# Kernel optimization log

Hardware: AMD Instinct MI355X
Metric: run time of the kernel (lower is better)

Reference implementation:

```python
import jax, jax.numpy as jnp
import numpy as np

C = 128        # in_channels
N = 80000      # nodes per type (user, item)
E = 1000000    # edges per relation
L = 400000     # link labels


def _evolve_gcn(x_src, edge_index, n_dst, p, W0, Wih, Whh, bih, bhh):
    """EvolveGCNH layer: TopK pooling -> 1-step GRU weight evolution -> GCN."""
    # TopK pooling: score = x @ p / ||p||, keep top C nodes, gate by tanh(score)
    score = x_src @ p / (jnp.linalg.norm(p) + 1e-16)          # [N_src]
    top_vals, top_idx = jax.lax.top_k(score, x_src.shape[1])   # k = C
    X_tilde = x_src[top_idx] * jnp.tanh(top_vals)[:, None]     # [C, C]
    # One GRU step: 'batch' dim = C rows of X_tilde, hidden = current weight W0
    gi = X_tilde @ Wih.T + bih                                 # [C, 3C]
    gh = W0 @ Whh.T + bhh                                      # [C, 3C]
    i_r, i_z, i_n = jnp.split(gi, 3, axis=1)
    h_r, h_z, h_n = jnp.split(gh, 3, axis=1)
    r = jax.nn.sigmoid(i_r + h_r)
    z = jax.nn.sigmoid(i_z + h_z)
    n = jnp.tanh(i_n + r * h_n)
    W = (1.0 - z) * n + z * W0                                 # evolved weight [C, C]
    # GCN propagation with symmetric degree norm, no self loops
    xw = x_src @ W                                             # [N_src, C]
    row, col = edge_index[0], edge_index[1]
    ones = jnp.ones(row.shape[0], dtype=xw.dtype)
    deg_src = jax.ops.segment_sum(ones, row, num_segments=x_src.shape[0])
    deg_dst = jax.ops.segment_sum(ones, col, num_segments=n_dst)
    inv_s = jnp.where(deg_src > 0, jax.lax.rsqrt(jnp.maximum(deg_src, 1.0)), 0.0)
    inv_d = jnp.where(deg_dst > 0, jax.lax.rsqrt(jnp.maximum(deg_dst, 1.0)), 0.0)
    norm = inv_s[row] * inv_d[col]                             # [E]
    return jax.ops.segment_sum(xw[row] * norm[:, None], col, num_segments=n_dst)


def setup_inputs() -> dict:
    key = jax.random.key(0)
    ks = jax.random.split(key, 20)
    f = lambda i, shape, s: jax.random.normal(ks[i], shape, dtype=jnp.float32) * s
    s_w = 1.0 / np.sqrt(C)
    return {
        "x_user": f(0, (N, C), 1.0),
        "x_item": f(1, (N, C), 1.0),
        "edge_ui": jax.random.randint(ks[2], (2, E), 0, N),
        "edge_iu": jax.random.randint(ks[3], (2, E), 0, N),
        "edge_label_index": jax.random.randint(ks[4], (2, L), 0, N),
        "p_ui": f(5, (C,), s_w),
        "W0_ui": f(6, (C, C), s_w),
        "Wih_ui": f(7, (3 * C, C), s_w),
        "Whh_ui": f(8, (3 * C, C), s_w),
        "bih_ui": f(9, (3 * C,), s_w),
        "bhh_ui": f(10, (3 * C,), s_w),
        "p_iu": f(11, (C,), s_w),
        "W0_iu": f(12, (C, C), s_w),
        "Wih_iu": f(13, (3 * C, C), s_w),
        "Whh_iu": f(14, (3 * C, C), s_w),
        "bih_iu": f(15, (3 * C,), s_w),
        "bhh_iu": f(16, (3 * C,), s_w),
        "W_post": f(17, (C, 2), s_w),
        "b_post": f(18, (2,), s_w),
    }


def reference(x_user, x_item, edge_ui, edge_iu, edge_label_index,
              p_ui, W0_ui, Wih_ui, Whh_ui, bih_ui, bhh_ui,
              p_iu, W0_iu, Wih_iu, Whh_iu, bih_iu, bhh_iu,
              W_post, b_post):
    # HeteroConv: one EvolveGCNH per relation, outputs grouped by dst node type
    h_item = jax.nn.relu(_evolve_gcn(x_user, edge_ui, x_item.shape[0],
                                     p_ui, W0_ui, Wih_ui, Whh_ui, bih_ui, bhh_ui))
    h_user = jax.nn.relu(_evolve_gcn(x_item, edge_iu, x_user.shape[0],
                                     p_iu, W0_iu, Wih_iu, Whh_iu, bih_iu, bhh_iu))
    # Link scorer: gather endpoints, hadamard, linear(C->2), sum over last dim
    h_src = h_user[edge_label_index[0]]                        # [L, C]
    h_dst = h_item[edge_label_index[1]]                        # [L, C]
    h = (h_src * h_dst) @ W_post + b_post                      # [L, 2]
    return jnp.sum(h, axis=-1)                                 # [L]
```

## Files before the change

### kernel.cpp

```cpp
#include <hip/hip_runtime.h>
#include <hip/hip_fp16.h>

constexpr int KC    = 128;
constexpr int NBLK  = 2048;
constexpr int CAPA  = 1024;
constexpr int CBITS = 12;
constexpr int CSZ   = 1 << CBITS;

using half8   = __attribute__((ext_vector_type(8))) _Float16;
using float4v = __attribute__((ext_vector_type(4))) float;

__device__ __forceinline__ unsigned fkey(float s) {
  unsigned u = __float_as_uint(s);
  return (u & 0x80000000u) ? ~u : (u | 0x80000000u);
}

__global__ __launch_bounds__(256) void m1_cnt_scores(
    const int* __restrict__ eui, const int* __restrict__ eiu,
    unsigned* __restrict__ cnts,
    const float* __restrict__ xu, const float* __restrict__ xi,
    const float* __restrict__ pu, const float* __restrict__ pi,
    float* __restrict__ scores, unsigned* __restrict__ hist,
    __half* __restrict__ x16,
    int E, int N, int NBC, int chunk, int NTOT) {
  __shared__ unsigned hD[4 * 48], hS[4 * 48];
  int t = threadIdx.x;
  if (blockIdx.x < NBLK) {
    int blk = blockIdx.x, w = t >> 6;
    for (int b = t; b < 4 * 48; b += 256) { hD[b] = 0; hS[b] = 0; }
    __syncthreads();
    int lo = blk * chunk, hi = min(2 * E, lo + chunk);
    for (int i = lo + t; i < hi; i += 256) {
      int rel = i >= E;
      const int* e = rel ? eiu : eui;
      int j = i - rel * E;
      atomicAdd(&hD[w * 48 + ((rel * N + e[E + j]) >> CBITS)], 1u);
      atomicAdd(&hS[w * 48 + ((rel * N + e[j]) >> CBITS)], 1u);
    }
    __syncthreads();
    for (int b = t; b < NBC; b += 256) {
      cnts[(size_t)blk * NBC + b] = hD[b] + hD[48 + b] + hD[96 + b] + hD[144 + b];
      cnts[(size_t)NTOT + (size_t)blk * NBC + b] =
          hS[b] + hS[48 + b] + hS[96 + b] + hS[144 + b];
    }
  } else {
    int gw = (blockIdx.x - NBLK) * 8 + (t >> 5);
    if (gw >= 2 * N) return;
    int lane = t & 31;
    int rel = gw >= N;
    int r = gw - rel * N;
    const float* x = rel ? xi : xu;
    const float* p = rel ? pi : pu;
    float4 xv = ((const float4*)(x + (size_t)r * KC))[lane];
    float4 pv = ((const float4*)p)[lane];
    __half2 h0 = __floats2half2_rn(xv.x, xv.y);
    __half2 h1 = __floats2half2_rn(xv.z, xv.w);
    uint2 u; u.x = *(unsigned*)&h0; u.y = *(unsigned*)&h1;
    ((uint2*)(x16 + (size_t)gw * KC))[lane] = u;
    float s = xv.x * pv.x + xv.y * pv.y + xv.z * pv.z + xv.w * pv.w;
#pragma unroll
    for (int off = 16; off; off >>= 1) s += __shfl_down(s, off, 32);
    if (lane == 0) {
      scores[gw] = s;
      atomicAdd(&hist[rel * 65536 + (fkey(s) >> 16)], 1u);
    }
  }
}

__global__ __launch_bounds__(1024) void m2_thresh_scan1(
    const unsigned* __restrict__ cnts, unsigned* __restrict__ sc,
    unsigned* __restrict__ bsum, const unsigned* __restrict__ hist,
    unsigned* __restrict__ ctrl, int NTOT, int NBC, int SCB) {
  __shared__ __align__(16) unsigned smem[1024 + 64 + 2];
  int t = threadIdx.x;
  if (blockIdx.x < 2) {
    const unsigned* h = hist + blockIdx.x * 65536;
    unsigned* c = ctrl + blockIdx.x * 8;
    unsigned* csum = smem;
    unsigned* bs = smem + 1024;
    unsigned s = 0;
    int hi = 65536 - 64 * t;
    for (int b = hi - 64; b < hi; ++b) s += h[b];
    csum[t] = s;
    __syncthreads();
    for (int off = 1; off < 1024; off <<= 1) {
      unsigned add = (t >= off) ? csum[t - off] : 0;
      __syncthreads();
      csum[t] += add;
      __syncthreads();
    }
    unsigned above = (t == 0) ? 0u : csum[t - 1];
    if (csum[t] >= 128u && above < 128u) { smem[1088] = (unsigned)t; smem[1089] = above; }
    __syncthreads();
    int chi = 65536 - 64 * (int)smem[1088];
    unsigned s_above = smem[1089];
    if (t < 64) bs[t] = h[chi - 1 - t];
    __syncthreads();
    if (t < 64) {
      unsigned v = bs[t], cum = v;
#pragma unroll
      for (int off = 1; off < 64; off <<= 1) {
        unsigned u = __shfl_up(cum, off, 64);
        if (t >= off) cum += u;
      }
      unsigned prev = cum - v;
      if (s_above + cum >= 128u && s_above + prev < 128u)
        c[0] = (unsigned)(chi - 1 - t);
    }
  } else {
    int vb = blockIdx.x - 2;
    unsigned* sh = smem;
    int seg = vb / SCB, lb = vb % SCB;
    int li = lb * 1024 + t;
    unsigned v = 0;
    if (li < NTOT) {
      int b = li >> 11, blk = li & (NBLK - 1);
      v = cnts[(size_t)seg * NTOT + (size_t)blk * NBC + b];
    }
    sh[t] = v; __syncthreads();
    for (int off = 1; off < 1024; off <<= 1) {
      unsigned add = (t >= off) ? sh[t - off] : 0;
      __syncthreads();
      sh[t] += add;
      __syncthreads();
    }
    if (li < NTOT) sc[(size_t)seg * NTOT + li] = sh[t] - v;
    if (t == 1023) bsum[vb] = sh[1023];
  }
}

__global__ __launch_bounds__(256) void m3_scan2_compact(
    unsigned* __restrict__ bsum, int nb,
    const float* __restrict__ scores, unsigned* __restrict__ ctrl,
    int* __restrict__ cand_idx, float* __restrict__ cand_val, int N) {
  if (blockIdx.x < 2) {
    __shared__ unsigned sh[256];
    unsigned* bs = bsum + blockIdx.x * nb;
    int t = threadIdx.x;
    unsigned v = (t < nb) ? bs[t] : 0;
    sh[t] = v; __syncthreads();
    for (int off = 1; off < 256; off <<= 1) {
      unsigned add = (t >= off) ? sh[t - off] : 0;
      __syncthreads();
      sh[t] += add;
      __syncthreads();
    }
    if (t < nb) bs[t] = sh[t] - v;
  } else {
    int i = (blockIdx.x - 2) * 256 + threadIdx.x;
    if (i >= 2 * N) return;
    int rel = i >= N;
    float s = scores[i];
    if ((fkey(s) >> 16) >= ctrl[rel * 8]) {
      unsigned pos = atomicAdd(&ctrl[rel * 8 + 1], 1u);
      if (pos < 2048u) {
        cand_idx[rel * 2048 + pos] = i - rel * N;
        cand_val[rel * 2048 + pos] = s;
      }
    }
  }
}

__global__ __launch_bounds__(256) void m4_topk_part(
    const int* __restrict__ eui, const int* __restrict__ eiu,
    const unsigned* __restrict__ cnts, const unsigned* __restrict__ sc,
    const unsigned* __restrict__ bsum,
    unsigned* __restrict__ recsD, unsigned* __restrict__ recsS,
    const unsigned* __restrict__ ctrl,
    const int* __restrict__ cand_idx, const float* __restrict__ cand_val,
    const float* __restrict__ pu, const float* __restrict__ pi,
    int* __restrict__ top_idx, float* __restrict__ top_tanh,
    int E, int N, int NBC, int chunk, int NTOT, int SCB) {
  __shared__ __align__(16) char smem[16896];
  int t = threadIdx.x;
  if (blockIdx.x < 2) {
    float* vals = (float*)smem;
    int*   idxs = (int*)(smem + 8192);
    float* red  = (float*)(smem + 16384);
    int rel = blockIdx.x;
    const float* p = rel ? pi : pu;
    int n = (int)ctrl[rel * 8 + 1]; if (n > 2048) n = 2048;
    for (int i = t; i < n; i += 256) {
      vals[i] = cand_val[rel * 2048 + i];
      idxs[i] = cand_idx[rel * 2048 + i];
    }
    if (t < 128) { float pv = p[t]; red[t] = pv * pv; }
    __syncthreads();
    for (int off = 64; off; off >>= 1) {
      if (t < off) red[t] += red[t + off];
      __syncthreads();
    }
    float pn = sqrtf(red[0]) + 1e-16f;
    for (int c = t; c < n; c += 256) {
      float v = vals[c]; int id = idxs[c];
      int rank = 0;
      for (int j = 0; j < n; ++j) {
        float vj = vals[j];
        rank += (vj > v) || (vj == v && idxs[j] < id);
      }
      if (rank < KC) {
        top_idx[rel * KC + rank] = id;
        top_tanh[rel * KC + rank] = tanhf(v / pn);
      }
    }
  } else {
    unsigned* curD   = (unsigned*)smem;
    unsigned* curS   = (unsigned*)(smem + 256);
    unsigned* deltaD = (unsigned*)(smem + 512);
    unsigned* deltaS = (unsigned*)(smem + 768);
    unsigned* stageD = (unsigned*)(smem + 1024);
    unsigned* stageS = (unsigned*)(smem + 5120);
    unsigned char* bktD = (unsigned char*)(smem + 9216);
    unsigned char* bktS = (unsigned char*)(smem + 10240);
    int blk = blockIdx.x - 2;
    if (t < 64) {
      unsigned v = (t < NBC) ? cnts[(size_t)blk * NBC + t] : 0;
      unsigned cum = v;
#pragma unroll
      for (int off = 1; off < 64; off <<= 1) {
        unsigned u = __shfl_up(cum, off, 64);
        if (t >= off) cum += u;
      }
      if (t < NBC) curD[t] = cum - v;
    } else if (t < 128) {
      int l = t - 64;
      unsigned v = (l < NBC) ? cnts[(size_t)NTOT + (size_t)blk * NBC + l] : 0;
      unsigned cum = v;
#pragma unroll
      for (int off = 1; off < 64; off <<= 1) {
        unsigned u = __shfl_up(cum, off, 64);
        if (l >= off) cum += u;
      }
      if (l < NBC) curS[l] = cum - v;
    }
    __syncthreads();
    if (t < NBC) {
      int li = t * NBLK + blk;
      deltaD[t] = sc[li] + bsum[li >> 10] - curD[t];
      deltaS[t] = sc[NTOT + li] + bsum[SCB + (li >> 10)] - curS[t];
    }
    __syncthreads();
    int lo = blk * chunk, hi = min(2 * E, lo + chunk);
    for (int i = lo + t; i < hi; i += 256) {
      int rel = i >= E;
      const int* e = rel ? eiu : eui;
      int j = i - rel * E;
      int src_g = rel * N + e[j];
      int dst_g = rel * N + e[E + j];
      int bD = dst_g >> CBITS;
      unsigned pD = atomicAdd(&curD[bD], 1u);
      stageD[pD] = (unsigned)src_g | ((unsigned)(dst_g & (CSZ - 1)) << 18);
      bktD[pD] = (unsigned char)bD;
      int bS = src_g >> CBITS;
      unsigned pS = atomicAdd(&curS[bS], 1u);
      stageS[pS] = (unsigned)(src_g & (CSZ - 1));
      bktS[pS] = (unsigned char)bS;
    }
    __syncthreads();
    int cnt = hi - lo;
    for (int j = t; j < cnt; j += 256) {
      recsD[deltaD[bktD[j]] + j] = stageD[j];
      recsS[deltaS[bktS[j]] + j] = stageS[j];
    }
  }
}

__global__ __launch_bounds__(1024) void m5_refine_gru(
    const unsigned* __restrict__ sc, const unsigned* __restrict__ bsum,
    const unsigned* __restrict__ recsD, const unsigned* __restrict__ recsS,
    int* __restrict__ ssrc, int* __restrict__ deg_dst, int* __restrict__ endp,
    int* __restrict__ deg_src,
    const float* __restrict__ xu, const float* __restrict__ xi,
    const int* __restrict__ top_idx, const float* __restrict__ top_tanh,
    const float* __restrict__ W0u, const float* __restrict__ W0i,
    const float* __restrict__ Wihu, const float* __restrict__ Wihi,
    const float* __restrict__ Whhu, const float* __restrict__ Whhi,
    const float* __restrict__ bihu, const float* __restrict__ bihi,
    const float* __restrict__ bhhu, const float* __restrict__ bhhi,
    __half* __restrict__ Wt,
    int E, int NBC, int N2, int NTOT, int SCB) {
  __shared__ __align__(16) char smem[32832];
  int t = threadIdx.x;
  if ((int)blockIdx.x < 2 * NBC) {
    unsigned* rh  = (unsigned*)smem;
    unsigned* cur = (unsigned*)(smem + 16384);
    unsigned* t16 = (unsigned*)(smem + 32768);
    int isS = blockIdx.x >= NBC;
    int c = blockIdx.x - (isS ? NBC : 0);
    size_t soff = isS ? (size_t)NTOT : 0;
    int bso = isS ? SCB : 0;
    int liLo = c * NBLK;
    int lo = (int)(sc[soff + liLo] + bsum[bso + (liLo >> 10)]);
    int hi;
    if (c + 1 < NBC) {
      int liHi = (c + 1) * NBLK;
      hi = (int)(sc[soff + liHi] + bsum[bso + (liHi >> 10)]);
    } else hi = 2 * E;
    for (int b = t; b < CSZ; b += 1024) rh[b] = 0;
    __syncthreads();
    if (isS) {
      for (int j = lo + t; j < hi; j += 1024)
        atomicAdd(&rh[recsS[j]], 1u);
      __syncthreads();
      for (int b = t; b < CSZ; b += 1024) {
        int node = c * CSZ + b;
        if (node < N2) deg_src[node] = (int)rh[b];
      }
    } else {
      for (int j = lo + t; j < hi; j += 1024)
        atomicAdd(&rh[recsD[j] >> 18], 1u);
      __syncthreads();
      unsigned loc[4], s = 0;
      int base = t * 4;
#pragma unroll
      for (int k = 0; k < 4; ++k) { unsigned v = rh[base + k]; loc[k] = s; s += v; }
      unsigned inc = s;
#pragma unroll
      for (int off = 1; off < 64; off <<= 1) {
        unsigned u = __shfl_up(inc, off, 64);
        if ((t & 63) >= off) inc += u;
      }
      int w = t >> 6;
      if ((t & 63) == 63) t16[w] = inc;
      __syncthreads();
      unsigned wbase = 0;
      for (int j = 0; j < 16; ++j) if (j < w) wbase += t16[j];
      unsigned exc = wbase + inc - s;
#pragma unroll
      for (int k = 0; k < 4; ++k) {
        unsigned e0 = exc + loc[k];
        cur[base + k] = e0;
        int node = c * CSZ + base + k;
        if (node < N2) {
          deg_dst[node] = (int)rh[base + k];
          endp[node] = lo + (int)(e0 + rh[base + k]);
        }
      }
      __syncthreads();
      for (int j = lo + t; j < hi; j += 1024) {
        unsigned rec = recsD[j];
        unsigned pos = atomicAdd(&cur[rec >> 18], 1u);
        ssrc[lo + (int)pos] = (int)(rec & 0x3FFFFu);
      }
    }
  } else {
    int gb = blockIdx.x - 2 * NBC;
    int rel = gb >> 7, c = gb & 127;
    const float* x   = rel ? xi   : xu;
    const float* W0  = rel ? W0i  : W0u;
    const float* Wih = rel ? Wihi : Wihu;
    const float* Whh = rel ? Whhi : Whhu;
    const float* bih = rel ? bihi : bihu;
    const float* bhh = rel ? bhhi : bhhu;
    float* xt = (float*)smem;
    float* w0 = (float*)(smem + 512);
    if (t < KC) {
      xt[t] = x[(size_t)top_idx[rel * KC + c] * KC + t] * top_tanh[rel * KC + c];
      w0[t] = W0[c * KC + t];
    }
    __syncthreads();
    if (t >= KC) return;
    int k = t;
    float gir = bih[k], giz = bih[KC + k], gin = bih[2 * KC + k];
    float ghr = bhh[k], ghz = bhh[KC + k], ghn = bhh[2 * KC + k];
    const float* wr = Wih + (size_t)k * KC;
    const float* wz = Wih + (size_t)(KC + k) * KC;
    const float* wn = Wih + (size_t)(2 * KC + k) * KC;
    const float* vr = Whh + (size_t)k * KC;
    const float* vz = Whh + (size_t)(KC + k) * KC;
    const float* vn = Whh + (size_t)(2 * KC + k) * KC;
    for (int j = 0; j < KC; ++j) {
      float xj = xt[j], hj = w0[j];
      gir += xj * wr[j]; giz += xj * wz[j]; gin += xj * wn[j];
      ghr += hj * vr[j]; ghz += hj * vz[j]; ghn += hj * vn[j];
    }
    float r = 1.f / (1.f + expf(-(gir + ghr)));
    float z = 1.f / (1.f + expf(-(giz + ghz)));
    float nn = tanhf(gin + r * ghn);
    float w = (1.f - z) * nn + z * w0[k];
    Wt[(size_t)rel * KC * KC + (size_t)k * KC + c] = __float2half_rn(w);
  }
}

__global__ __launch_bounds__(256) void k_gemm(const __half* __restrict__ x16,
                                              const __half* __restrict__ Wt,
                                              const int* __restrict__ deg_src,
                                              __half* __restrict__ xw, int N) {
  __shared__ __half Ws[KC * KC];
  __shared__ __half outs[64 * 136];
  int rel = (blockIdx.x * 64) >= N;
  int t = threadIdx.x;
  const uint4* wg = (const uint4*)(Wt + (size_t)rel * KC * KC);
#pragma unroll
  for (int i = 0; i < 8; ++i)
    ((uint4*)Ws)[t + 256 * i] = wg[t + 256 * i];
  __syncthreads();
  int wid = t >> 6, lane = t & 63;
  int l15 = lane & 15, quad = lane >> 4;
  int row0 = blockIdx.x * 64 + wid * 16;
  half8 a[4];
  const __half* xrow = x16 + (size_t)(row0 + l15) * KC + quad * 8;
#pragma unroll
  for (int ks = 0; ks < 4; ++ks) a[ks] = *(const half8*)(xrow + ks * 32);
  float4v acc[8];
#pragma unroll
  for (int nt = 0; nt < 8; ++nt) {
    acc[nt] = (float4v){0.f, 0.f, 0.f, 0.f};
#pragma unroll
    for (int ks = 0; ks < 4; ++ks) {
      half8 b = *(const half8*)&Ws[(nt * 16 + l15) * KC + ks * 32 + quad * 8];
      acc[nt] = __builtin_amdgcn_mfma_f32_16x16x32_f16(a[ks], b, acc[nt], 0, 0, 0);
    }
  }
  float scv[4];
#pragma unroll
  for (int r = 0; r < 4; ++r) {
    int dg = deg_src[row0 + quad * 4 + r];
    scv[r] = dg > 0 ? rsqrtf((float)dg) : 0.f;
  }
  __half* ob = outs + (size_t)wid * 16 * 136;
#pragma unroll
  for (int nt = 0; nt < 8; ++nt)
#pragma unroll
    for (int r = 0; r < 4; ++r)
      ob[(quad * 4 + r) * 136 + nt * 16 + l15] = __float2half_rn(acc[nt][r] * scv[r]);
  __syncthreads();
  size_t gbase = (size_t)blockIdx.x * 64 * KC;
#pragma unroll
  for (int i = 0; i < 4; ++i) {
    int idx = t + 256 * i;
    int rr = idx >> 4, cc = idx & 15;
    *(uint4*)(xw + gbase + (size_t)rr * KC + cc * 8) =
        *(const uint4*)(outs + (size_t)rr * 136 + cc * 8);
  }
}

__global__ void k_agg(const __half* __restrict__ xw, const int* __restrict__ ssrc,
                      const int* __restrict__ endp, const int* __restrict__ deg_dst,
                      __half* __restrict__ h, int n2) {
  int gw = (int)((blockIdx.x * blockDim.x + threadIdx.x) >> 6);
  if (gw >= n2) return;
  int lane = threadIdx.x & 63;
  int q = lane >> 4, l16 = lane & 15;
  int d = deg_dst[gw];
  int end = endp[gw], start = end - d;
  __half2 z = __floats2half2_rn(0.f, 0.f);
  __half2 a0[4], a1[4], a2[4], a3[4];
#pragma unroll
  for (int k = 0; k < 4; ++k) { a0[k] = z; a1[k] = z; a2[k] = z; a3[k] = z; }
  for (int i = start + q; i < end; i += 16) {
    int i1 = i + 4, i2 = i + 8, i3 = i + 12;
    bool b1 = i1 < end, b2 = i2 < end, b3 = i3 < end;
    int r0 = ssrc[i], r1, r2, r3;
    if (b1) r1 = ssrc[i1];
    if (b2) r2 = ssrc[i2];
    if (b3) r3 = ssrc[i3];
    uint4 u0 = ((const uint4*)(xw + (size_t)r0 * KC))[l16];
    uint4 u1, u2, u3;
    if (b1) u1 = ((const uint4*)(xw + (size_t)r1 * KC))[l16];
    if (b2) u2 = ((const uint4*)(xw + (size_t)r2 * KC))[l16];
    if (b3) u3 = ((const uint4*)(xw + (size_t)r3 * KC))[l16];
    {
      const __half2* p = (const __half2*)&u0;
#pragma unroll
      for (int k = 0; k < 4; ++k) a0[k] = __hadd2(a0[k], p[k]);
    }
    if (b1) {
      const __half2* p = (const __half2*)&u1;
#pragma unroll
      for (int k = 0; k < 4; ++k) a1[k] = __hadd2(a1[k], p[k]);
    }
    if (b2) {
      const __half2* p = (const __half2*)&u2;
#pragma unroll
      for (int k = 0; k < 4; ++k) a2[k] = __hadd2(a2[k], p[k]);
    }
    if (b3) {
      const __half2* p = (const __half2*)&u3;
#pragma unroll
      for (int k = 0; k < 4; ++k) a3[k] = __hadd2(a3[k], p[k]);
    }
  }
  float f[8];
#pragma unroll
  for (int k = 0; k < 4; ++k) {
    float2 x0 = __half22float2(a0[k]);
    float2 x1 = __half22float2(a1[k]);
    float2 x2 = __half22float2(a2[k]);
    float2 x3 = __half22float2(a3[k]);
    f[2 * k]     = (x0.x + x1.x) + (x2.x + x3.x);
    f[2 * k + 1] = (x0.y + x1.y) + (x2.y + x3.y);
  }
#pragma unroll
  for (int k = 0; k < 8; ++k) {
    f[k] += __shfl_xor(f[k], 16, 64);
    f[k] += __shfl_xor(f[k], 32, 64);
  }
  if (q == 0) {
    float invd = d > 0 ? rsqrtf((float)d) : 0.f;
    __half2 pk[4];
#pragma unroll
    for (int k = 0; k < 4; ++k)
      pk[k] = __floats2half2_rn(fmaxf(f[2 * k] * invd, 0.f),
                                fmaxf(f[2 * k + 1] * invd, 0.f));
    uint4 u;
    u.x = *(unsigned*)&pk[0]; u.y = *(unsigned*)&pk[1];
    u.z = *(unsigned*)&pk[2]; u.w = *(unsigned*)&pk[3];
    ((uint4*)(h + (size_t)gw * KC))[l16] = u;
  }
}

__global__ void k_links(const __half* __restrict__ h,
                        const int* __restrict__ srcs, const int* __restrict__ dsts,
                        const float* __restrict__ Wp, const float* __restrict__ bp,
                        float* __restrict__ out, int L, int N) {
  int tid = blockIdx.x * blockDim.x + threadIdx.x;
  int lane = threadIdx.x & 63;
  int q = lane >> 4, l16 = lane & 15;
  int gq = (tid >> 6) * 4 + q;
  int nq = (int)((gridDim.x * blockDim.x) >> 6) * 4;
  float w8[8];
#pragma unroll
  for (int k = 0; k < 4; ++k) {
    float4 w = ((const float4*)Wp)[l16 * 4 + k];
    w8[2 * k] = w.x + w.y; w8[2 * k + 1] = w.z + w.w;
  }
  float bs = bp[0] + bp[1];
  const __half* hu = h + (size_t)N * KC;
  for (int li = gq; li < L; li += nq) {
    int s = srcs[li], dd = dsts[li];
    uint4 ua = ((const uint4*)(hu + (size_t)s * KC))[l16];
    uint4 ub = ((const uint4*)(h + (size_t)dd * KC))[l16];
    const __half2* pa = (const __half2*)&ua;
    const __half2* pb = (const __half2*)&ub;
    float acc = 0.f;
#pragma unroll
    for (int k = 0; k < 4; ++k) {
      float2 fa = __half22float2(pa[k]);
      float2 fb = __half22float2(pb[k]);
      acc += fa.x * fb.x * w8[2 * k] + fa.y * fb.y * w8[2 * k + 1];
    }
#pragma unroll
    for (int off = 8; off; off >>= 1) acc += __shfl_xor(acc, off, 64);
    if (l16 == 0) out[li] = acc + bs;
  }
}

extern "C" void kernel_launch(void* const* d_in, const int* in_sizes, int n_in,
                              void* d_out, int out_size, void* d_ws, size_t ws_size,
                              hipStream_t stream) {
  const float* x_user = (const float*)d_in[0];
  const float* x_item = (const float*)d_in[1];
  const int*   edge_ui = (const int*)d_in[2];
  const int*   edge_iu = (const int*)d_in[3];
  const int*   elab    = (const int*)d_in[4];
  const float* p_ui   = (const float*)d_in[5];
  const float* W0_ui  = (const float*)d_in[6];
  const float* Wih_ui = (const float*)d_in[7];
  const float* Whh_ui = (const float*)d_in[8];
  const float* bih_ui = (const float*)d_in[9];
  const float* bhh_ui = (const float*)d_in[10];
  const float* p_iu   = (const float*)d_in[11];
  const float* W0_iu  = (const float*)d_in[12];
  const float* Wih_iu = (const float*)d_in[13];
  const float* Whh_iu = (const float*)d_in[14];
  const float* bih_iu = (const float*)d_in[15];
  const float* bhh_iu = (const float*)d_in[16];
  const float* W_post = (const float*)d_in[17];
  const float* b_post = (const float*)d_in[18];
  const int N = in_sizes[0] / KC;
  const int E = in_sizes[2] / 2;
  const int L = in_sizes[4] / 2;
  const int N2 = 2 * N;
  const int NBC = (N2 + CSZ - 1) >> CBITS;
  const int chunk = (2 * E + NBLK - 1) / NBLK;
  const int NTOT = NBC * NBLK;
  const int SCB = (NTOT + 1023) / 1024;

  char* wsp = (char*)d_ws;
  auto carve = [&](size_t bytes) -> void* {
    void* p = (void*)wsp;
    wsp += (bytes + 255) & ~(size_t)255;
    return p;
  };
  const size_t histB = 2 * 65536 * 4;
  const size_t zBytes = histB + 256;
  char*     zbase    = (char*)carve(zBytes);
  unsigned* hist     = (unsigned*)zbase;
  unsigned* ctrl     = (unsigned*)(zbase + histB);
  int*      deg_src  = (int*)carve((size_t)N2 * 4);
  __half*   x16      = (__half*)carve((size_t)N2 * KC * 2);
  __half*   xw       = (__half*)carve((size_t)N2 * KC * 2);
  __half*   h        = (__half*)carve((size_t)N2 * KC * 2);
  float*    scores   = (float*)carve((size_t)N2 * 4);
  int*      cand_idx = (int*)carve(2 * 2048 * 4);
  float*    cand_val = (float*)carve(2 * 2048 * 4);
  int*      top_idx  = (int*)carve(2 * KC * 4);
  float*    top_tanh = (float*)carve(2 * KC * 4);
  __half*   Wt16     = (__half*)carve(2 * KC * KC * 2);
  unsigned* cnts     = (unsigned*)carve((size_t)2 * NTOT * 4);
  unsigned* sc       = (unsigned*)carve((size_t)2 * NTOT * 4);
  unsigned* bsum     = (unsigned*)carve((size_t)2 * SCB * 4);
  unsigned* recsD    = (unsigned*)carve((size_t)2 * E * 4);
  unsigned* recsS    = (unsigned*)carve((size_t)2 * E * 4);
  int*      ssrc     = (int*)carve((size_t)2 * E * 4);
  int*      deg_dst  = (int*)carve((size_t)N2 * 4);
  int*      endp     = (int*)carve((size_t)N2 * 4);

  hipMemsetAsync(zbase, 0, zBytes, stream);

  const int SBLK = (N2 + 7) / 8;
  m1_cnt_scores<<<NBLK + SBLK, 256, 0, stream>>>(edge_ui, edge_iu, cnts,
                                                 x_user, x_item, p_ui, p_iu,
                                                 scores, hist, x16,
                                                 E, N, NBC, chunk, NTOT);
  m2_thresh_scan1<<<2 + 2 * SCB, 1024, 0, stream>>>(cnts, sc, bsum, hist, ctrl,
                                                    NTOT, NBC, SCB);
  m3_scan2_compact<<<2 + (N2 + 255) / 256, 256, 0, stream>>>(bsum, SCB, scores, ctrl,
                                                             cand_idx, cand_val, N);
  m4_topk_part<<<2 + NBLK, 256, 0, stream>>>(edge_ui, edge_iu, cnts, sc, bsum,
                                             recsD, recsS, ctrl, cand_idx, cand_val,
                                             p_ui, p_iu, top_idx, top_tanh,
                                             E, N, NBC, chunk, NTOT, SCB);
  m5_refine_gru<<<2 * NBC + 2 * KC, 1024, 0, stream>>>(sc, bsum, recsD, recsS, ssrc,
                                                       deg_dst, endp, deg_src,
                                                       x_user, x_item, top_idx, top_tanh,
                                                       W0_ui, W0_iu, Wih_ui, Wih_iu,
                                                       Whh_ui, Whh_iu, bih_ui, bih_iu,
                                                       bhh_ui, bhh_iu, Wt16,
                                                       E, NBC, N2, NTOT, SCB);
  k_gemm<<<N2 / 64, 256, 0, stream>>>(x16, Wt16, deg_src, xw, N);
  k_agg<<<(N2 + 3) / 4, 256, 0, stream>>>(xw, ssrc, endp, deg_dst, h, N2);
  k_links<<<2048, 256, 0, stream>>>(h, elab, elab + L, W_post, b_post,
                                    (float*)d_out, L, N);
}
```

Measured before the change: 424.9 us.

## Compute source degrees with global atomics and shrink dst buckets to 1024 nodes

Source-degree counting moves out of the bucketed counting-sort pipeline and becomes direct global atomicAdd into a zeroed deg_src array in the first kernel. This drops the recsS records, their scan, the scatter and the refine pass. Destination buckets shrink from 4096 to 1024 nodes, so there are more, smaller refine blocks, each with one histogram entry per thread. This cuts memory traffic and scan work, at the cost of about 2M random global atomics and a larger per-block bucket histogram and scan.

```diff
diff --git a/kernel.cpp b/kernel.cpp
--- a/kernel.cpp
+++ b/kernel.cpp
@@ -4,8 +4,9 @@
 constexpr int KC    = 128;
 constexpr int NBLK  = 2048;
 constexpr int CAPA  = 1024;
-constexpr int CBITS = 12;
+constexpr int CBITS = 10;
 constexpr int CSZ   = 1 << CBITS;
+constexpr int NBCM  = 192;
 
 using half8   = __attribute__((ext_vector_type(8))) _Float16;
 using float4v = __attribute__((ext_vector_type(4))) float;
@@ -17,32 +18,30 @@
 
 __global__ __launch_bounds__(256) void m1_cnt_scores(
     const int* __restrict__ eui, const int* __restrict__ eiu,
-    unsigned* __restrict__ cnts,
+    unsigned* __restrict__ cnts, int* __restrict__ deg_src,
     const float* __restrict__ xu, const float* __restrict__ xi,
     const float* __restrict__ pu, const float* __restrict__ pi,
     float* __restrict__ scores, unsigned* __restrict__ hist,
     __half* __restrict__ x16,
-    int E, int N, int NBC, int chunk, int NTOT) {
-  __shared__ unsigned hD[4 * 48], hS[4 * 48];
+    int E, int N, int NBC, int chunk) {
+  __shared__ unsigned hD[4 * NBCM];
   int t = threadIdx.x;
   if (blockIdx.x < NBLK) {
     int blk = blockIdx.x, w = t >> 6;
-    for (int b = t; b < 4 * 48; b += 256) { hD[b] = 0; hS[b] = 0; }
+    for (int b = t; b < 4 * NBCM; b += 256) hD[b] = 0;
     __syncthreads();
     int lo = blk * chunk, hi = min(2 * E, lo + chunk);
     for (int i = lo + t; i < hi; i += 256) {
       int rel = i >= E;
       const int* e = rel ? eiu : eui;
       int j = i - rel * E;
-      atomicAdd(&hD[w * 48 + ((rel * N + e[E + j]) >> CBITS)], 1u);
-      atomicAdd(&hS[w * 48 + ((rel * N + e[j]) >> CBITS)], 1u);
-    }
-    __syncthreads();
-    for (int b = t; b < NBC; b += 256) {
-      cnts[(size_t)blk * NBC + b] = hD[b] + hD[48 + b] + hD[96 + b] + hD[144 + b];
-      cnts[(size_t)NTOT + (size_t)blk * NBC + b] =
-          hS[b] + hS[48 + b] + hS[96 + b] + hS[144 + b];
-    }
+      atomicAdd(&hD[w * NBCM + ((rel * N + e[E + j]) >> CBITS)], 1u);
+      atomicAdd(&deg_src[rel * N + e[j]], 1);
+    }
+    __syncthreads();
+    for (int b = t; b < NBC; b += 256)
+      cnts[(size_t)blk * NBC + b] =
+          hD[b] + hD[NBCM + b] + hD[2 * NBCM + b] + hD[3 * NBCM + b];
   } else {
     int gw = (blockIdx.x - NBLK) * 8 + (t >> 5);
     if (gw >= 2 * N) return;
@@ -70,7 +69,7 @@
 __global__ __launch_bounds__(1024) void m2_thresh_scan1(
     const unsigned* __restrict__ cnts, unsigned* __restrict__ sc,
     unsigned* __restrict__ bsum, const unsigned* __restrict__ hist,
-    unsigned* __restrict__ ctrl, int NTOT, int NBC, int SCB) {
+    unsigned* __restrict__ ctrl, int NTOT, int NBC) {
   __shared__ __align__(16) unsigned smem[1024 + 64 + 2];
   int t = threadIdx.x;
   if (blockIdx.x < 2) {
@@ -110,12 +109,11 @@
   } else {
     int vb = blockIdx.x - 2;
     unsigned* sh = smem;
-    int seg = vb / SCB, lb = vb % SCB;
-    int li = lb * 1024 + t;
+    int li = vb * 1024 + t;
     unsigned v = 0;
     if (li < NTOT) {
       int b = li >> 11, blk = li & (NBLK - 1);
-      v = cnts[(size_t)seg * NTOT + (size_t)blk * NBC + b];
+      v = cnts[(size_t)blk * NBC + b];
     }
     sh[t] = v; __syncthreads();
     for (int off = 1; off < 1024; off <<= 1) {
@@ -124,30 +122,29 @@
       sh[t] += add;
       __syncthreads();
     }
-    if (li < NTOT) sc[(size_t)seg * NTOT + li] = sh[t] - v;
+    if (li < NTOT) sc[li] = sh[t] - v;
     if (t == 1023) bsum[vb] = sh[1023];
   }
 }
 
-__global__ __launch_bounds__(256) void m3_scan2_compact(
+__global__ __launch_bounds__(512) void m3_scan2_compact(
     unsigned* __restrict__ bsum, int nb,
     const float* __restrict__ scores, unsigned* __restrict__ ctrl,
     int* __restrict__ cand_idx, float* __restrict__ cand_val, int N) {
-  if (blockIdx.x < 2) {
-    __shared__ unsigned sh[256];
-    unsigned* bs = bsum + blockIdx.x * nb;
+  if (blockIdx.x == 0) {
+    __shared__ unsigned sh[512];
     int t = threadIdx.x;
-    unsigned v = (t < nb) ? bs[t] : 0;
+    unsigned v = (t < nb) ? bsum[t] : 0;
     sh[t] = v; __syncthreads();
-    for (int off = 1; off < 256; off <<= 1) {
+    for (int off = 1; off < 512; off <<= 1) {
       unsigned add = (t >= off) ? sh[t - off] : 0;
       __syncthreads();
       sh[t] += add;
       __syncthreads();
     }
-    if (t < nb) bs[t] = sh[t] - v;
+    if (t < nb) bsum[t] = sh[t] - v;
   } else {
-    int i = (blockIdx.x - 2) * 256 + threadIdx.x;
+    int i = (blockIdx.x - 1) * 512 + threadIdx.x;
     if (i >= 2 * N) return;
     int rel = i >= N;
     float s = scores[i];
@@ -165,12 +162,12 @@
     const int* __restrict__ eui, const int* __restrict__ eiu,
     const unsigned* __restrict__ cnts, const unsigned* __restrict__ sc,
     const unsigned* __restrict__ bsum,
-    unsigned* __restrict__ recsD, unsigned* __restrict__ recsS,
+    unsigned* __restrict__ recsD,
     const unsigned* __restrict__ ctrl,
     const int* __restrict__ cand_idx, const float* __restrict__ cand_val,
     const float* __restrict__ pu, const float* __restrict__ pi,
     int* __restrict__ top_idx, float* __restrict__ top_tanh,
-    int E, int N, int NBC, int chunk, int NTOT, int SCB) {
+    int E, int N, int NBC, int chunk) {
   __shared__ __align__(16) char smem[16896];
   int t = threadIdx.x;
   if (blockIdx.x < 2) {
@@ -204,40 +201,25 @@
       }
     }
   } else {
-    unsigned* curD   = (unsigned*)smem;
-    unsigned* curS   = (unsigned*)(smem + 256);
-    unsigned* deltaD = (unsigned*)(smem + 512);
-    unsigned* deltaS = (unsigned*)(smem + 768);
-    unsigned* stageD = (unsigned*)(smem + 1024);
-    unsigned* stageS = (unsigned*)(smem + 5120);
-    unsigned char* bktD = (unsigned char*)(smem + 9216);
-    unsigned char* bktS = (unsigned char*)(smem + 10240);
+    unsigned* scn    = (unsigned*)smem;
+    unsigned* curD   = (unsigned*)(smem + 1024);
+    unsigned* deltaD = (unsigned*)(smem + 2048);
+    unsigned* stageD = (unsigned*)(smem + 3072);
+    unsigned char* bktD = (unsigned char*)(smem + 7168);
     int blk = blockIdx.x - 2;
-    if (t < 64) {
-      unsigned v = (t < NBC) ? cnts[(size_t)blk * NBC + t] : 0;
-      unsigned cum = v;
-#pragma unroll
-      for (int off = 1; off < 64; off <<= 1) {
-        unsigned u = __shfl_up(cum, off, 64);
-        if (t >= off) cum += u;
-      }
-      if (t < NBC) curD[t] = cum - v;
-    } else if (t < 128) {
-      int l = t - 64;
-      unsigned v = (l < NBC) ? cnts[(size_t)NTOT + (size_t)blk * NBC + l] : 0;
-      unsigned cum = v;
-#pragma unroll
-      for (int off = 1; off < 64; off <<= 1) {
-        unsigned u = __shfl_up(cum, off, 64);
-        if (l >= off) cum += u;
-      }
-      if (l < NBC) curS[l] = cum - v;
-    }
-    __syncthreads();
+    unsigned v = (t < NBC) ? cnts[(size_t)blk * NBC + t] : 0;
+    scn[t] = v; __syncthreads();
+    for (int off = 1; off < 256; off <<= 1) {
+      unsigned add = (t >= off) ? scn[t - off] : 0;
+      __syncthreads();
+      scn[t] += add;
+      __syncthreads();
+    }
     if (t < NBC) {
+      unsigned exc = scn[t] - v;
+      curD[t] = exc;
       int li = t * NBLK + blk;
-      deltaD[t] = sc[li] + bsum[li >> 10] - curD[t];
-      deltaS[t] = sc[NTOT + li] + bsum[SCB + (li >> 10)] - curS[t];
+      deltaD[t] = sc[li] + bsum[li >> 10] - exc;
     }
     __syncthreads();
     int lo = blk * chunk, hi = min(2 * E, lo + chunk);
@@ -251,25 +233,18 @@
       unsigned pD = atomicAdd(&curD[bD], 1u);
       stageD[pD] = (unsigned)src_g | ((unsigned)(dst_g & (CSZ - 1)) << 18);
       bktD[pD] = (unsigned char)bD;
-      int bS = src_g >> CBITS;
-      unsigned pS = atomicAdd(&curS[bS], 1u);
-      stageS[pS] = (unsigned)(src_g & (CSZ - 1));
-      bktS[pS] = (unsigned char)bS;
     }
     __syncthreads();
     int cnt = hi - lo;
-    for (int j = t; j < cnt; j += 256) {
+    for (int j = t; j < cnt; j += 256)
       recsD[deltaD[bktD[j]] + j] = stageD[j];
-      recsS[deltaS[bktS[j]] + j] = stageS[j];
-    }
   }
 }
 
 __global__ __launch_bounds__(1024) void m5_refine_gru(
     const unsigned* __restrict__ sc, const unsigned* __restrict__ bsum,
-    const unsigned* __restrict__ recsD, const unsigned* __restrict__ recsS,
+    const unsigned* __restrict__ recsD,
     int* __restrict__ ssrc, int* __restrict__ deg_dst, int* __restrict__ endp,
-    int* __restrict__ deg_src,
     const float* __restrict__ xu, const float* __restrict__ xi,
     const int* __restrict__ top_idx, const float* __restrict__ top_tanh,
     const float* __restrict__ W0u, const float* __restrict__ W0i,
@@ -278,73 +253,53 @@
     const float* __restrict__ bihu, const float* __restrict__ bihi,
     const float* __restrict__ bhhu, const float* __restrict__ bhhi,
     __half* __restrict__ Wt,
-    int E, int NBC, int N2, int NTOT, int SCB) {
-  __shared__ __align__(16) char smem[32832];
+    int E, int NBC, int N2) {
+  __shared__ __align__(16) char smem[8256];
   int t = threadIdx.x;
-  if ((int)blockIdx.x < 2 * NBC) {
-    unsigned* rh  = (unsigned*)smem;
-    unsigned* cur = (unsigned*)(smem + 16384);
-    unsigned* t16 = (unsigned*)(smem + 32768);
-    int isS = blockIdx.x >= NBC;
-    int c = blockIdx.x - (isS ? NBC : 0);
-    size_t soff = isS ? (size_t)NTOT : 0;
-    int bso = isS ? SCB : 0;
+  if ((int)blockIdx.x < NBC) {
+    unsigned* hist = (unsigned*)smem;
+    unsigned* cur  = (unsigned*)(smem + 4096);
+    unsigned* t16  = (unsigned*)(smem + 8192);
+    int c = blockIdx.x;
     int liLo = c * NBLK;
-    int lo = (int)(sc[soff + liLo] + bsum[bso + (liLo >> 10)]);
+    int lo = (int)(sc[liLo] + bsum[liLo >> 10]);
     int hi;
     if (c + 1 < NBC) {
       int liHi = (c + 1) * NBLK;
-      hi = (int)(sc[soff + liHi] + bsum[bso + (liHi >> 10)]);
+      hi = (int)(sc[liHi] + bsum[liHi >> 10]);
     } else hi = 2 * E;
-    for (int b = t; b < CSZ; b += 1024) rh[b] = 0;
-    __syncthreads();
-    if (isS) {
-      for (int j = lo + t; j < hi; j += 1024)
-        atomicAdd(&rh[recsS[j]], 1u);
-      __syncthreads();
-      for (int b = t; b < CSZ; b += 1024) {
-        int node = c * CSZ + b;
-        if (node < N2) deg_src[node] = (int)rh[b];
-      }
-    } else {
-      for (int j = lo + t; j < hi; j += 1024)
-        atomicAdd(&rh[recsD[j] >> 18], 1u);
-      __syncthreads();
-      unsigned loc[4], s = 0;
-      int base = t * 4;
-#pragma unroll
-      for (int k = 0; k < 4; ++k) { unsigned v = rh[base + k]; loc[k] = s; s += v; }
-      unsigned inc = s;
-#pragma unroll
-      for (int off = 1; off < 64; off <<= 1) {
-        unsigned u = __shfl_up(inc, off, 64);
-        if ((t & 63) >= off) inc += u;
-      }
-      int w = t >> 6;
-      if ((t & 63) == 63) t16[w] = inc;
-      __syncthreads();
-      unsigned wbase = 0;
-      for (int j = 0; j < 16; ++j) if (j < w) wbase += t16[j];
-      unsigned exc = wbase + inc - s;
-#pragma unroll
-      for (int k = 0; k < 4; ++k) {
-        unsigned e0 = exc + loc[k];
-        cur[base + k] = e0;
-        int node = c * CSZ + base + k;
-        if (node < N2) {
-          deg_dst[node] = (int)rh[base + k];
-          endp[node] = lo + (int)(e0 + rh[base + k]);
-        }
-      }
-      __syncthreads();
-      for (int j = lo + t; j < hi; j += 1024) {
-        unsigned rec = recsD[j];
-        unsigned pos = atomicAdd(&cur[rec >> 18], 1u);
-        ssrc[lo + (int)pos] = (int)(rec & 0x3FFFFu);
-      }
+    hist[t] = 0;
+    __syncthreads();
+    for (int j = lo + t; j < hi; j += 1024)
+      atomicAdd(&hist[recsD[j] >> 18], 1u);
+    __syncthreads();
+    unsigned v = hist[t];
+    unsigned inc = v;
+#pragma unroll
+    for (int off = 1; off < 64; off <<= 1) {
+      unsigned u = __shfl_up(inc, off, 64);
+      if ((t & 63) >= off) inc += u;
+    }
+    int w = t >> 6;
+    if ((t & 63) == 63) t16[w] = inc;
+    __syncthreads();
+    unsigned wbase = 0;
+    for (int j = 0; j < 16; ++j) if (j < w) wbase += t16[j];
+    unsigned exc = wbase + inc - v;
+    cur[t] = exc;
+    int node = c * CSZ + t;
+    if (node < N2) {
+      deg_dst[node] = (int)v;
+      endp[node] = lo + (int)(exc + v);
+    }
+    __syncthreads();
+    for (int j = lo + t; j < hi; j += 1024) {
+      unsigned rec = recsD[j];
+      unsigned pos = atomicAdd(&cur[rec >> 18], 1u);
+      ssrc[lo + (int)pos] = (int)(rec & 0x3FFFFu);
     }
   } else {
-    int gb = blockIdx.x - 2 * NBC;
+    int gb = blockIdx.x - NBC;
     int rel = gb >> 7, c = gb & 127;
     const float* x   = rel ? xi   : xu;
     const float* W0  = rel ? W0i  : W0u;
@@ -584,11 +539,11 @@
     return p;
   };
   const size_t histB = 2 * 65536 * 4;
-  const size_t zBytes = histB + 256;
+  const size_t zBytes = histB + 256 + (size_t)N2 * 4;
   char*     zbase    = (char*)carve(zBytes);
   unsigned* hist     = (unsigned*)zbase;
   unsigned* ctrl     = (unsigned*)(zbase + histB);
-  int*      deg_src  = (int*)carve((size_t)N2 * 4);
+  int*      deg_src  = (int*)(zbase + histB + 256);
   __half*   x16      = (__half*)carve((size_t)N2 * KC * 2);
   __half*   xw       = (__half*)carve((size_t)N2 * KC * 2);
   __half*   h        = (__half*)carve((size_t)N2 * KC * 2);
@@ -598,11 +553,10 @@
   int*      top_idx  = (int*)carve(2 * KC * 4);
   float*    top_tanh = (float*)carve(2 * KC * 4);
   __half*   Wt16     = (__half*)carve(2 * KC * KC * 2);
-  unsigned* cnts     = (unsigned*)carve((size_t)2 * NTOT * 4);
-  unsigned* sc       = (unsigned*)carve((size_t)2 * NTOT * 4);
-  unsigned* bsum     = (unsigned*)carve((size_t)2 * SCB * 4);
+  unsigned* cnts     = (unsigned*)carve((size_t)NTOT * 4);
+  unsigned* sc       = (unsigned*)carve((size_t)NTOT * 4);
+  unsigned* bsum     = (unsigned*)carve((size_t)SCB * 4);
   unsigned* recsD    = (unsigned*)carve((size_t)2 * E * 4);
-  unsigned* recsS    = (unsigned*)carve((size_t)2 * E * 4);
   int*      ssrc     = (int*)carve((size_t)2 * E * 4);
   int*      deg_dst  = (int*)carve((size_t)N2 * 4);
   int*      endp     = (int*)carve((size_t)N2 * 4);
@@ -610,25 +564,25 @@
   hipMemsetAsync(zbase, 0, zBytes, stream);
 
   const int SBLK = (N2 + 7) / 8;
-  m1_cnt_scores<<<NBLK + SBLK, 256, 0, stream>>>(edge_ui, edge_iu, cnts,
+  m1_cnt_scores<<<NBLK + SBLK, 256, 0, stream>>>(edge_ui, edge_iu, cnts, deg_src,
                                                  x_user, x_item, p_ui, p_iu,
                                                  scores, hist, x16,
-                                                 E, N, NBC, chunk, NTOT);
-  m2_thresh_scan1<<<2 + 2 * SCB, 1024, 0, stream>>>(cnts, sc, bsum, hist, ctrl,
-                                                    NTOT, NBC, SCB);
-  m3_scan2_compact<<<2 + (N2 + 255) / 256, 256, 0, stream>>>(bsum, SCB, scores, ctrl,
+                                                 E, N, NBC, chunk);
+  m2_thresh_scan1<<<2 + SCB, 1024, 0, stream>>>(cnts, sc, bsum, hist, ctrl,
+                                                NTOT, NBC);
+  m3_scan2_compact<<<1 + (N2 + 511) / 512, 512, 0, stream>>>(bsum, SCB, scores, ctrl,
                                                              cand_idx, cand_val, N);
   m4_topk_part<<<2 + NBLK, 256, 0, stream>>>(edge_ui, edge_iu, cnts, sc, bsum,
-                                             recsD, recsS, ctrl, cand_idx, cand_val,
+                                             recsD, ctrl, cand_idx, cand_val,
                                              p_ui, p_iu, top_idx, top_tanh,
-                                             E, N, NBC, chunk, NTOT, SCB);
-  m5_refine_gru<<<2 * NBC + 2 * KC, 1024, 0, stream>>>(sc, bsum, recsD, recsS, ssrc,
-                                                       deg_dst, endp, deg_src,
-                                                       x_user, x_item, top_idx, top_tanh,
-                                                       W0_ui, W0_iu, Wih_ui, Wih_iu,
-                                                       Whh_ui, Whh_iu, bih_ui, bih_iu,
-                                                       bhh_ui, bhh_iu, Wt16,
-                                                       E, NBC, N2, NTOT, SCB);
+                                             E, N, NBC, chunk);
+  m5_refine_gru<<<NBC + 2 * KC, 1024, 0, stream>>>(sc, bsum, recsD, ssrc,
+                                                   deg_dst, endp,
+                                                   x_user, x_item, top_idx, top_tanh,
+                                                   W0_ui, W0_iu, Wih_ui, Wih_iu,
+                                                   Whh_ui, Whh_iu, bih_ui, bih_iu,
+                                                   bhh_ui, bhh_iu, Wt16,
+                                                   E, NBC, N2);
   k_gemm<<<N2 / 64, 256, 0, stream>>>(x16, Wt16, deg_src, xw, N);
   k_agg<<<(N2 + 3) / 4, 256, 0, stream>>>(xw, ssrc, endp, deg_dst, h, N2);
   k_links<<<2048, 256, 0, stream>>>(h, elab, elab + L, W_post, b_post,
```

Result: slower. 458.4 us (+7.9%).
